# Performance work log

Measured on AMD Instinct MI355X. Metric: run time of the kernel, lower is better.

## Reference

```python
import jax, jax.numpy as jnp
import numpy as np

B, T, P, D, H = 16, 512, 576, 1024, 16
HD = D // H  # head_dim = 64
SCALE = 1.0 / np.sqrt(HD).astype(np.float32)


def _split_heads(x):
    # [B, S, D] -> [B, H, S, HD]
    b, s, _ = x.shape
    return x.reshape(b, s, H, HD).transpose(0, 2, 1, 3)


def _merge_heads(x):
    # [B, H, S, HD] -> [B, S, D]
    b, h, s, hd = x.shape
    return x.transpose(0, 2, 1, 3).reshape(b, s, h * hd)


def _linear(x, w, b):
    # torch nn.Linear: y = x @ W^T + b, W is [out, in]
    return jnp.einsum('bsd,od->bso', x, w) + b


def setup_inputs() -> dict:
    key = jax.random.key(0)
    ks = jax.random.split(key, 12)
    inp = {
        'text_feats': jax.random.normal(ks[0], (B, T, D), jnp.float32),
        'image_feats': jax.random.normal(ks[1], (B, P, D), jnp.float32),
        'text_mask': jnp.ones((B, T), dtype=bool),
    }
    names = ['qt', 'ki', 'vi', 'qi', 'kt', 'vt', 'ot', 'oi']
    for i, n in enumerate(names):
        inp['w_' + n] = jax.random.normal(ks[2 + i], (D, D), jnp.float32) * 0.02
        inp['b_' + n] = jnp.zeros((D,), jnp.float32)
    return inp


def reference(text_feats, image_feats, text_mask,
              w_qt, b_qt, w_ki, b_ki, w_vi, b_vi,
              w_qi, b_qi, w_kt, b_kt, w_vt, b_vt,
              w_ot, b_ot, w_oi, b_oi):
    # ---- text attends to image (no mask on image keys) ----
    q_t = _split_heads(_linear(text_feats, w_qt, b_qt))    # [B,H,T,HD]
    k_i = _split_heads(_linear(image_feats, w_ki, b_ki))   # [B,H,P,HD]
    v_i = _split_heads(_linear(image_feats, w_vi, b_vi))   # [B,H,P,HD]
    scores_ti = jnp.einsum('bhtd,bhpd->bhtp', q_t, k_i) * SCALE
    attn_ti = jax.nn.softmax(scores_ti, axis=-1)
    text_attended = _merge_heads(jnp.einsum('bhtp,bhpd->bhtd', attn_ti, v_i))
    text_attended = _linear(text_attended, w_ot, b_ot)

    # ---- image attends to text (mask on text keys) ----
    q_i = _split_heads(_linear(image_feats, w_qi, b_qi))   # [B,H,P,HD]
    k_t = _split_heads(_linear(text_feats, w_kt, b_kt))    # [B,H,T,HD]
    v_t = _split_heads(_linear(text_feats, w_vt, b_vt))    # [B,H,T,HD]
    scores_it = jnp.einsum('bhpd,bhtd->bhpt', q_i, k_t) * SCALE
    scores_it = jnp.where(text_mask[:, None, None, :], scores_it, -jnp.inf)
    attn_it = jax.nn.softmax(scores_it, axis=-1)
    image_attended = _merge_heads(jnp.einsum('bhpt,bhtd->bhpd', attn_it, v_t))
    image_attended = _linear(image_attended, w_oi, b_oi)

    return (text_attended, image_attended)
```

## Files before the change

### kernel.cpp

```cpp
#include <hip/hip_runtime.h>
#include <stdint.h>

typedef unsigned short u16;
typedef __bf16 bf16x8 __attribute__((ext_vector_type(8)));
typedef float f32x4 __attribute__((ext_vector_type(4)));

#define SCALE_QK 0.125f

__device__ __forceinline__ u16 f2bf(float f) {
    uint32_t u = __builtin_bit_cast(uint32_t, f);
    u += 0x7FFFu + ((u >> 16) & 1u);
    return (u16)(u >> 16);
}

__device__ __forceinline__ int bdiv(int x, int S) {
    return (S == 512) ? (x >> 9) : (int)(((uint64_t)(x >> 6) * 954437177ull) >> 33);
}

__device__ __forceinline__ void gload16(const void* g, void* l) {
    __builtin_amdgcn_global_load_lds(
        (__attribute__((address_space(1))) void*)(g),
        (__attribute__((address_space(3))) void*)(l), 16, 0, 0);
}

template<int W>
__device__ __forceinline__ void vwait() {
    asm volatile("s_waitcnt vmcnt(%0)" :: "n"(W) : "memory");
}

__global__ void cvt_f32_bf16(const float* __restrict__ src, u16* __restrict__ dst, int n4) {
    int i = blockIdx.x * blockDim.x + threadIdx.x;
    if (i >= n4) return;
    float4 v = ((const float4*)src)[i];
    ushort4 o;
    o.x = f2bf(v.x); o.y = f2bf(v.y); o.z = f2bf(v.z); o.w = f2bf(v.w);
    ((ushort4*)dst)[i] = o;
}

struct Ptr8 { const float* p[8]; };

__global__ void cvt_w8(Ptr8 srcs, u16* __restrict__ dst) {
    int i = blockIdx.x * blockDim.x + threadIdx.x;
    int mat = i >> 18, off = i & 262143;
    float4 v = ((const float4*)srcs.p[mat])[off];
    ushort4 o;
    o.x = f2bf(v.x); o.y = f2bf(v.y); o.z = f2bf(v.z); o.w = f2bf(v.w);
    ((ushort4*)(dst + ((size_t)mat << 20)))[off] = o;
}

__global__ void prep(const int* __restrict__ maski, float* __restrict__ mb,
                     const float* __restrict__ bqt, const float* __restrict__ bkt,
                     const float* __restrict__ bqi, const float* __restrict__ bki,
                     float* __restrict__ biasbuf) {
    int i = blockIdx.x * blockDim.x + threadIdx.x;
    if (i < 8192) {
        int v0 = maski[0];
        int v = (v0 == 0x01010101) ? (int)((const unsigned char*)maski)[i] : maski[i];
        mb[i] = v ? 0.0f : -1e30f;
    } else if (i < 12288) {
        int j = i - 8192;
        float v = (j < 1024) ? bqt[j] : (j < 2048) ? bkt[j - 1024]
                : (j < 3072) ? bqi[j - 2048] : bki[j - 3072];
        biasbuf[j] = v;
    }
}

struct Seg {
    const u16* A; const u16* B; const float* bias; void* C;
    int nx, S, layout, end; size_t pstr;
};
struct Segs { Seg s[4]; };

__global__ __launch_bounds__(512, 2)
void gemm256v2(Segs segs) {
    constexpr int K = 1024;
    __shared__ u16 U[4][256 * 64];
    const int tid = threadIdx.x;
    const int wid = tid >> 6, lane = tid & 63;
    const int lo = lane & 15, hi = lane >> 4;
    const int wm = wid >> 2, wn = wid & 3;
    const int tot = (int)gridDim.x;
    int f = ((int)blockIdx.x & 7) * (tot >> 3) + ((int)blockIdx.x >> 3);
    int si = 0;
    while (si < 3 && f >= segs.s[si].end) ++si;
    if (si > 0) f -= segs.s[si - 1].end;
    const Seg sg = segs.s[si];
    const int bm = f / sg.nx, bn = f - bm * sg.nx;
    const u16* Ab = sg.A + (size_t)bm * 256 * K;
    const u16* Bb = sg.B + (size_t)bn * 256 * K;

    const int srow8 = tid >> 3;
    const int sslot = tid & 7;

    auto stage_unit = [&](int u) {
        const int reg = u & 3;
        const int kb = u * 32;
#pragma unroll
        for (int c = 0; c < 4; ++c) {
            int row = c * 64 + srow8;
            int ss = sslot ^ (row & 7);
            const u16* src = (ss < 4)
                ? Ab + (size_t)row * K + kb + ss * 8
                : Bb + (size_t)row * K + kb + (ss - 4) * 8;
            gload16(src, &U[reg][0] + c * 4096 + wid * 512);
        }
    };

    f32x4 acc[8][4] = {};

    stage_unit(0); stage_unit(1); stage_unit(2);

    auto phase = [&](int u, bool doStage) {
        const u16* R = &U[u & 3][0];
        bf16x8 af[8], bq[4];
#pragma unroll
        for (int m = 0; m < 8; ++m) {
            int row = wm * 128 + m * 16 + lo;
            af[m] = *(const bf16x8*)(R + row * 64 + ((hi ^ (row & 7)) << 3));
        }
#pragma unroll
        for (int n = 0; n < 4; ++n) {
            int row = wn * 64 + n * 16 + lo;
            bq[n] = *(const bf16x8*)(R + row * 64 + (((4 + hi) ^ (row & 7)) << 3));
        }
        if (doStage) stage_unit(u + 3);
        __builtin_amdgcn_s_setprio(1);
#pragma unroll
        for (int m = 0; m < 8; ++m)
#pragma unroll
            for (int n = 0; n < 4; ++n)
                acc[m][n] = __builtin_amdgcn_mfma_f32_16x16x32_bf16(af[m], bq[n], acc[m][n], 0, 0, 0);
        __builtin_amdgcn_s_setprio(0);
    };

#pragma unroll 4
    for (int u = 0; u < 28; ++u) {
        vwait<8>();
        __builtin_amdgcn_s_barrier();
        phase(u, true);
    }
    vwait<8>(); __builtin_amdgcn_s_barrier(); phase(28, true);
    vwait<8>(); __builtin_amdgcn_s_barrier(); phase(29, false);
    vwait<4>(); __builtin_amdgcn_s_barrier(); phase(30, false);
    vwait<0>(); __builtin_amdgcn_s_barrier(); phase(31, false);

    const int rowbase = bm * 256 + wm * 128, colbase = bn * 256 + wn * 64;

    if (sg.layout == 0) {
        float* C = (float*)sg.C;
#pragma unroll
        for (int m = 0; m < 8; ++m)
#pragma unroll
            for (int r = 0; r < 4; ++r) {
                int row = rowbase + m * 16 + hi * 4 + r;
#pragma unroll
                for (int n = 0; n < 4; ++n) {
                    int col = colbase + n * 16 + lo;
                    C[(size_t)row * 1024 + col] = acc[m][n][r] + sg.bias[col];
                }
            }
    } else if (sg.layout == 1) {
#pragma unroll
        for (int m = 0; m < 8; ++m)
#pragma unroll
            for (int r = 0; r < 4; ++r) {
                int row = rowbase + m * 16 + hi * 4 + r;
                int b = bdiv(row, sg.S);
                int s = row - b * sg.S;
#pragma unroll
                for (int n = 0; n < 4; ++n) {
                    int cb = colbase + n * 16;
                    int part = cb >> 10, h = (cb >> 6) & 15;
                    u16* bp = (u16*)sg.C + (size_t)part * sg.pstr +
                              (((size_t)(b * 16 + h) * sg.S + s) << 6) + (cb & 63) + lo;
                    *bp = f2bf(acc[m][n][r] + sg.bias[cb + lo]);
                }
            }
    } else {
        u16* base = (u16*)sg.C;
        int bn_[4], s0_[4];
#pragma unroll
        for (int n = 0; n < 4; ++n) {
            int col0 = colbase + n * 16;
            int b = bdiv(col0, sg.S);
            bn_[n] = b;
            s0_[n] = col0 - b * sg.S;
        }
#pragma unroll
        for (int m = 0; m < 8; ++m)
#pragma unroll
            for (int r = 0; r < 4; ++r) {
                int dout = rowbase + m * 16 + hi * 4 + r;
                float bv = sg.bias[dout];
#pragma unroll
                for (int n = 0; n < 4; ++n)
                    base[((size_t)bn_[n] * 1024 + dout) * sg.S + s0_[n] + lo] =
                        f2bf(acc[m][n][r] + bv);
            }
    }
}

template<int MASKED, int NQ, int SK>
__global__ __launch_bounds__(256)
void attn_v4(const u16* __restrict__ Q, const u16* __restrict__ Kb,
             const u16* __restrict__ Vt, const float* __restrict__ mb,
             u16* __restrict__ Out) {
    constexpr int SQ = NQ * 64;
    constexpr int NC = SK / 64;
    __shared__ u16 kls[2][64 * 64];
    __shared__ u16 vls[2][64 * 64];
    __shared__ u16 pls[4][16 * 72];
    const int tid = threadIdx.x, wid = tid >> 6, lane = tid & 63;
    const int lo = lane & 15, hi = lane >> 4;
    const int id = blockIdx.x;
    const int f = (id & 7) * (NQ * 32) + (id >> 3);
    const int qc = f % NQ, bh = f / NQ;
    const int b = bh >> 4, h = bh & 15;
    const int q0 = qc * 64 + wid * 16;
    const u16* Qp = Q + ((size_t)bh * SQ + q0) * 64;
    const u16* Kp = Kb + (size_t)bh * SK * 64;
    const u16* Vp = Vt + (size_t)bh * 64 * SK;

    bf16x8 qf[2];
#pragma unroll
    for (int ks = 0; ks < 2; ++ks)
        qf[ks] = *(const bf16x8*)(Qp + lo * 64 + ks * 32 + hi * 8);

    f32x4 oacc[4] = {};
    float m = -3e38f, l = 0.f;
    u16* pl = pls[wid];
    uint32_t* pl32 = (uint32_t*)pl;

    auto stage = [&](int bufi, int c0) {
#pragma unroll
        for (int j = 0; j < 2; ++j) {
            const int beta = (j * 4 + wid) * 64 + lane;
            const int row = beta >> 3, slot = beta & 7;
            const int e = (slot ^ (row & 7)) << 3;
            gload16(Kp + (size_t)(c0 + row) * 64 + e,
                    &kls[bufi][0] + (j * 4 + wid) * 512);
            gload16(Vp + (size_t)row * SK + c0 + e,
                    &vls[bufi][0] + (j * 4 + wid) * 512);
        }
    };

    stage(0, 0);
    __syncthreads();

    for (int c = 0; c < NC; ++c) {
        const int c0 = c * 64;
        if (c + 1 < NC) stage((c + 1) & 1, c0 + 64);
        const u16* kb = &kls[c & 1][0];
        const u16* vb = &vls[c & 1][0];

        float sc[4][4];
#pragma unroll
        for (int kt = 0; kt < 4; ++kt) {
            const int krow = kt * 16 + lo;
            const int rx = krow & 7;
            bf16x8 kf0 = *(const bf16x8*)(kb + krow * 64 + ((hi ^ rx) << 3));
            bf16x8 kf1 = *(const bf16x8*)(kb + krow * 64 + (((4 + hi) ^ rx) << 3));
            f32x4 z = {};
            __builtin_amdgcn_s_setprio(1);
            z = __builtin_amdgcn_mfma_f32_16x16x32_bf16(kf0, qf[0], z, 0, 0, 0);
            z = __builtin_amdgcn_mfma_f32_16x16x32_bf16(kf1, qf[1], z, 0, 0, 0);
            __builtin_amdgcn_s_setprio(0);
            if (MASKED) {
                float4 mv = *(const float4*)(mb + b * SK + c0 + kt * 16 + hi * 4);
#pragma unroll
                for (int r = 0; r < 4; ++r) sc[kt][r] = z[r] * SCALE_QK + ((const float*)&mv)[r];
            } else {
#pragma unroll
                for (int r = 0; r < 4; ++r) sc[kt][r] = z[r] * SCALE_QK;
            }
        }
        float a0 = fmaxf(fmaxf(sc[0][0], sc[0][1]), fmaxf(sc[0][2], sc[0][3]));
        float a1 = fmaxf(fmaxf(sc[1][0], sc[1][1]), fmaxf(sc[1][2], sc[1][3]));
        float a2 = fmaxf(fmaxf(sc[2][0], sc[2][1]), fmaxf(sc[2][2], sc[2][3]));
        float a3 = fmaxf(fmaxf(sc[3][0], sc[3][1]), fmaxf(sc[3][2], sc[3][3]));
        float pmax = fmaxf(fmaxf(a0, a1), fmaxf(a2, a3));
        pmax = fmaxf(pmax, __shfl_xor(pmax, 16));
        pmax = fmaxf(pmax, __shfl_xor(pmax, 32));
        if (!__all(pmax - m <= 8.0f)) {
            float mn = fmaxf(m, pmax);
            float alpha = __expf(m - mn);
            m = mn;
            l *= alpha;
#pragma unroll
            for (int n = 0; n < 4; ++n)
#pragma unroll
                for (int r = 0; r < 4; ++r) oacc[n][r] *= alpha;
        }
        float sum = 0.f;
#pragma unroll
        for (int kt = 0; kt < 4; ++kt) {
#pragma unroll
            for (int r = 0; r < 4; ++r) {
                float p = __expf(sc[kt][r] - m);
                sc[kt][r] = p;
                sum += p;
            }
        }
        sum += __shfl_xor(sum, 16);
        sum += __shfl_xor(sum, 32);
        l += sum;
#pragma unroll
        for (int kt = 0; kt < 4; ++kt) {
#pragma unroll
            for (int rp = 0; rp < 2; ++rp) {
                uint32_t w = (uint32_t)f2bf(sc[kt][2 * rp]) |
                             ((uint32_t)f2bf(sc[kt][2 * rp + 1]) << 16);
                pl32[lo * 36 + kt * 8 + hi * 2 + rp] = w;
            }
        }
        bf16x8 pf0 = *(const bf16x8*)(pl + lo * 72 + hi * 8);
        bf16x8 pf1 = *(const bf16x8*)(pl + lo * 72 + 32 + hi * 8);
        __builtin_amdgcn_s_setprio(1);
#pragma unroll
        for (int n = 0; n < 4; ++n) {
            const int d = n * 16 + lo;
            const int dx = d & 7;
            bf16x8 v0 = *(const bf16x8*)(vb + d * 64 + ((hi ^ dx) << 3));
            bf16x8 v1 = *(const bf16x8*)(vb + d * 64 + (((4 + hi) ^ dx) << 3));
            oacc[n] = __builtin_amdgcn_mfma_f32_16x16x32_bf16(v0, pf0, oacc[n], 0, 0, 0);
            oacc[n] = __builtin_amdgcn_mfma_f32_16x16x32_bf16(v1, pf1, oacc[n], 0, 0, 0);
        }
        __builtin_amdgcn_s_setprio(0);
        __syncthreads();
    }
    const float inv = 1.0f / l;
    u16* op = Out + ((size_t)(b * SQ + q0 + lo)) * 1024 + h * 64;
#pragma unroll
    for (int n = 0; n < 4; ++n) {
        ushort4 w;
        w.x = f2bf(oacc[n][0] * inv);
        w.y = f2bf(oacc[n][1] * inv);
        w.z = f2bf(oacc[n][2] * inv);
        w.w = f2bf(oacc[n][3] * inv);
        *(ushort4*)(op + n * 16 + hi * 4) = w;
    }
}

extern "C" void kernel_launch(void* const* d_in, const int* in_sizes, int n_in,
                              void* d_out, int out_size, void* d_ws, size_t ws_size,
                              hipStream_t stream) {
    (void)in_sizes; (void)n_in; (void)out_size; (void)ws_size;
    const float* text  = (const float*)d_in[0];
    const float* image = (const float*)d_in[1];
    const int*   maski = (const int*)d_in[2];
    const float* w_qt = (const float*)d_in[3];  const float* b_qt = (const float*)d_in[4];
    const float* w_ki = (const float*)d_in[5];  const float* b_ki = (const float*)d_in[6];
    const float* w_vi = (const float*)d_in[7];  const float* b_vi = (const float*)d_in[8];
    const float* w_qi = (const float*)d_in[9];  const float* b_qi = (const float*)d_in[10];
    const float* w_kt = (const float*)d_in[11]; const float* b_kt = (const float*)d_in[12];
    const float* w_vt = (const float*)d_in[13]; const float* b_vt = (const float*)d_in[14];
    const float* w_ot = (const float*)d_in[15]; const float* b_ot = (const float*)d_in[16];
    const float* w_oi = (const float*)d_in[17]; const float* b_oi = (const float*)d_in[18];

    const int B = 16, T = 512, P = 576, D = 1024;
    const int MT = B * T;
    const int MI = B * P;
    const size_t M1 = 1 << 20;

    char* wp = (char*)d_ws;
    auto alloc = [&](size_t bytes) { char* r = wp; wp += (bytes + 255) & ~(size_t)255; return r; };
    u16* Xt   = (u16*)alloc((size_t)MT * D * 2);
    u16* Xi   = (u16*)alloc((size_t)MI * D * 2);
    u16* Wall = (u16*)alloc(8 * M1 * 2);
    float* biasbuf = (float*)alloc(4096 * 4);
    float* mbf  = (float*)alloc((size_t)B * T * 4);
    u16* QKt  = (u16*)alloc((size_t)2 * MT * D * 2);
    u16* QKi  = (u16*)alloc((size_t)2 * MI * D * 2);
    u16* Vtt  = (u16*)alloc((size_t)MT * D * 2);
    u16* Vti  = (u16*)alloc((size_t)MI * D * 2);

    const u16* Wqk_t = Wall;
    const u16* Wqk_i = Wall + 2 * M1;
    const u16* Wv_t  = Wall + 4 * M1;
    const u16* Wv_i  = Wall + 5 * M1;
    const u16* Wot   = Wall + 6 * M1;
    const u16* Woi   = Wall + 7 * M1;

    cvt_f32_bf16<<<(MT * D / 4) / 256, 256, 0, stream>>>(text, Xt, MT * D / 4);
    cvt_f32_bf16<<<(MI * D / 4) / 256, 256, 0, stream>>>(image, Xi, MI * D / 4);
    Ptr8 w8 = {{w_qt, w_kt, w_qi, w_ki, w_vt, w_vi, w_ot, w_oi}};
    cvt_w8<<<8192, 256, 0, stream>>>(w8, Wall);
    prep<<<48, 256, 0, stream>>>(maski, mbf, b_qt, b_kt, b_qi, b_ki, biasbuf);

    {
        Segs sgs;
        sgs.s[0] = {Xt,   Wqk_t, biasbuf,        QKt, 8,  512, 1, 256, (size_t)MT * D};
        sgs.s[1] = {Xi,   Wqk_i, biasbuf + 2048, QKi, 8,  576, 1, 544, (size_t)MI * D};
        sgs.s[2] = {Wv_t, Xt,    b_vt,           Vtt, 32, 512, 2, 672, 0};
        sgs.s[3] = {Wv_i, Xi,    b_vi,           Vti, 36, 576, 2, 816, 0};
        gemm256v2<<<816, 512, 0, stream>>>(sgs);
    }

    attn_v4<0, 8, 576><<<8 * 256, 256, 0, stream>>>(
        QKt, QKi + (size_t)MI * D, Vti, nullptr, Xt);
    attn_v4<1, 9, 512><<<9 * 256, 256, 0, stream>>>(
        QKi, QKt + (size_t)MT * D, Vtt, mbf, Xi);

    {
        Segs sgs;
        sgs.s[0] = {Xt, Wot, b_ot, d_out, 4, 512, 0, 128, 0};
        sgs.s[1] = {Xi, Woi, b_oi, (void*)((float*)d_out + (size_t)MT * D), 4, 576, 0, 272, 0};
        sgs.s[2] = sgs.s[1]; sgs.s[2].end = 272;
        sgs.s[3] = sgs.s[1]; sgs.s[3].end = 272;
        gemm256v2<<<272, 512, 0, stream>>>(sgs);
    }
}
```

Before: 358.3 us.

## Restructure GEMM mainloop to double-buffered 64-wide K tiles with split stages

Replaces the 4-stage ring of 32-wide K units (A and B packed in one buffer) with separate A and B double buffers holding 64-wide K tiles. Each tile is consumed in four sub-phases, with the next tile's loads spread across them. This halves the pipeline depth, drops the minimum-occupancy launch bound, and halves the A fragment registers per phase. It adds more barriers per tile and gives less prefetch lead time, which may expose global load latency.

```diff
diff --git a/kernel.cpp b/kernel.cpp
--- a/kernel.cpp
+++ b/kernel.cpp
@@ -71,10 +71,12 @@
 };
 struct Segs { Seg s[4]; };
 
-__global__ __launch_bounds__(512, 2)
-void gemm256v2(Segs segs) {
+__global__ __launch_bounds__(512)
+void gemm256v3(Segs segs) {
     constexpr int K = 1024;
-    __shared__ u16 U[4][256 * 64];
+    constexpr int NT = 16;
+    __shared__ u16 As[2][256 * 64];
+    __shared__ u16 Bs[2][256 * 64];
     const int tid = threadIdx.x;
     const int wid = tid >> 6, lane = tid & 63;
     const int lo = lane & 15, hi = lane >> 4;
@@ -89,60 +91,71 @@
     const u16* Ab = sg.A + (size_t)bm * 256 * K;
     const u16* Bb = sg.B + (size_t)bn * 256 * K;
 
-    const int srow8 = tid >> 3;
+    const int srow = tid >> 3;
     const int sslot = tid & 7;
 
-    auto stage_unit = [&](int u) {
-        const int reg = u & 3;
-        const int kb = u * 32;
-#pragma unroll
-        for (int c = 0; c < 4; ++c) {
-            int row = c * 64 + srow8;
-            int ss = sslot ^ (row & 7);
-            const u16* src = (ss < 4)
-                ? Ab + (size_t)row * K + kb + ss * 8
-                : Bb + (size_t)row * K + kb + (ss - 4) * 8;
-            gload16(src, &U[reg][0] + c * 4096 + wid * 512);
-        }
+    auto stageA = [&](int buf, int t1, int c) {
+        int row = c * 64 + srow;
+        int ss = sslot ^ (row & 7);
+        gload16(Ab + (size_t)row * K + t1 * 64 + ss * 8,
+                &As[buf][0] + c * 4096 + wid * 512);
     };
+    auto stageB = [&](int buf, int t1, int c) {
+        int row = c * 64 + srow;
+        int ss = sslot ^ (row & 7);
+        gload16(Bb + (size_t)row * K + t1 * 64 + ss * 8,
+                &Bs[buf][0] + c * 4096 + wid * 512);
+    };
 
     f32x4 acc[8][4] = {};
 
-    stage_unit(0); stage_unit(1); stage_unit(2);
-
-    auto phase = [&](int u, bool doStage) {
-        const u16* R = &U[u & 3][0];
-        bf16x8 af[8], bq[4];
-#pragma unroll
-        for (int m = 0; m < 8; ++m) {
-            int row = wm * 128 + m * 16 + lo;
-            af[m] = *(const bf16x8*)(R + row * 64 + ((hi ^ (row & 7)) << 3));
-        }
-#pragma unroll
-        for (int n = 0; n < 4; ++n) {
-            int row = wn * 64 + n * 16 + lo;
-            bq[n] = *(const bf16x8*)(R + row * 64 + (((4 + hi) ^ (row & 7)) << 3));
-        }
-        if (doStage) stage_unit(u + 3);
-        __builtin_amdgcn_s_setprio(1);
-#pragma unroll
-        for (int m = 0; m < 8; ++m)
-#pragma unroll
-            for (int n = 0; n < 4; ++n)
-                acc[m][n] = __builtin_amdgcn_mfma_f32_16x16x32_bf16(af[m], bq[n], acc[m][n], 0, 0, 0);
-        __builtin_amdgcn_s_setprio(0);
-    };
-
-#pragma unroll 4
-    for (int u = 0; u < 28; ++u) {
-        vwait<8>();
-        __builtin_amdgcn_s_barrier();
-        phase(u, true);
-    }
-    vwait<8>(); __builtin_amdgcn_s_barrier(); phase(28, true);
-    vwait<8>(); __builtin_amdgcn_s_barrier(); phase(29, false);
-    vwait<4>(); __builtin_amdgcn_s_barrier(); phase(30, false);
-    vwait<0>(); __builtin_amdgcn_s_barrier(); phase(31, false);
+    stageB(0, 0, 0); stageB(0, 0, 1); stageB(0, 0, 2); stageB(0, 0, 3);
+    stageA(0, 0, 0); stageA(0, 0, 2); stageA(0, 0, 1); stageA(0, 0, 3);
+    vwait<2>();
+    __builtin_amdgcn_s_barrier();
+
+    for (int t = 0; t < NT; ++t) {
+        const int cur = t & 1;
+        const u16* At = &As[cur][0];
+        const u16* Bt = &Bs[cur][0];
+        const bool st = (t + 1 < NT);
+#pragma unroll
+        for (int ph = 0; ph < 4; ++ph) {
+            const int ks = ph >> 1, mh = ph & 1;
+            bf16x8 af[4], bq[4];
+#pragma unroll
+            for (int m = 0; m < 4; ++m) {
+                int row = wm * 128 + mh * 64 + m * 16 + lo;
+                af[m] = *(const bf16x8*)(At + row * 64 + (((ks * 4 + hi) ^ (row & 7)) << 3));
+            }
+#pragma unroll
+            for (int n = 0; n < 4; ++n) {
+                int row = wn * 64 + n * 16 + lo;
+                bq[n] = *(const bf16x8*)(Bt + row * 64 + (((ks * 4 + hi) ^ (row & 7)) << 3));
+            }
+            if (st) {
+                if (ph == 0)      { stageB(cur ^ 1, t + 1, 0); stageB(cur ^ 1, t + 1, 1); }
+                else if (ph == 1) { stageB(cur ^ 1, t + 1, 2); stageB(cur ^ 1, t + 1, 3); }
+                else if (ph == 2) { stageA(cur ^ 1, t + 1, 0); stageA(cur ^ 1, t + 1, 2); }
+                else              { stageA(cur ^ 1, t + 1, 1); stageA(cur ^ 1, t + 1, 3); }
+            }
+            __builtin_amdgcn_s_barrier();
+            __builtin_amdgcn_s_setprio(1);
+#pragma unroll
+            for (int m = 0; m < 4; ++m)
+#pragma unroll
+                for (int n = 0; n < 4; ++n)
+                    acc[mh * 4 + m][n] =
+                        __builtin_amdgcn_mfma_f32_16x16x32_bf16(af[m], bq[n], acc[mh * 4 + m][n], 0, 0, 0);
+            __builtin_amdgcn_s_setprio(0);
+            if (ph == 0) {
+                if (st) vwait<2>(); else vwait<0>();
+            } else if (ph == 3) {
+                vwait<2>();
+            }
+            __builtin_amdgcn_s_barrier();
+        }
+    }
 
     const int rowbase = bm * 256 + wm * 128, colbase = bn * 256 + wn * 64;
 
@@ -393,7 +406,7 @@
         sgs.s[1] = {Xi,   Wqk_i, biasbuf + 2048, QKi, 8,  576, 1, 544, (size_t)MI * D};
         sgs.s[2] = {Wv_t, Xt,    b_vt,           Vtt, 32, 512, 2, 672, 0};
         sgs.s[3] = {Wv_i, Xi,    b_vi,           Vti, 36, 576, 2, 816, 0};
-        gemm256v2<<<816, 512, 0, stream>>>(sgs);
+        gemm256v3<<<816, 512, 0, stream>>>(sgs);
     }
 
     attn_v4<0, 8, 576><<<8 * 256, 256, 0, stream>>>(
@@ -407,6 +420,6 @@
         sgs.s[1] = {Xi, Woi, b_oi, (void*)((float*)d_out + (size_t)MT * D), 4, 576, 0, 272, 0};
         sgs.s[2] = sgs.s[1]; sgs.s[2].end = 272;
         sgs.s[3] = sgs.s[1]; sgs.s[3].end = 272;
-        gemm256v2<<<272, 512, 0, stream>>>(sgs);
-    }
-}
+        gemm256v3<<<272, 512, 0, stream>>>(sgs);
+    }
+}
```

After: 377.4 us. 5.3% more time.

## Restructure GEMM main loop into double-buffered pairs with precomputed addresses

Applied to the files above, without the earlier changes.

The GEMM pipeline changes from a 4-slot ring with three stages in flight and partial vmcnt waits to a pair-based double buffer. Each step waits for all loads, computes two K-slices, and issues loads for the next pair between them. Global source pointers and LDS read offsets are now computed once instead of per unit, which cuts address arithmetic. The min-blocks-per-CU hint of 2 is also dropped. Waiting on vmcnt(0) every step leaves less load overlap than the old deeper prefetch, so memory latency may be less well hidden.

```diff
diff --git a/kernel.cpp b/kernel.cpp
--- a/kernel.cpp
+++ b/kernel.cpp
@@ -71,10 +71,10 @@
 };
 struct Segs { Seg s[4]; };
 
-__global__ __launch_bounds__(512, 2)
-void gemm256v2(Segs segs) {
+__global__ __launch_bounds__(512)
+void gemm256v4(Segs segs) {
     constexpr int K = 1024;
-    __shared__ u16 U[4][256 * 64];
+    __shared__ u16 U[4][16384];
     const int tid = threadIdx.x;
     const int wid = tid >> 6, lane = tid & 63;
     const int lo = lane & 15, hi = lane >> 4;
@@ -89,41 +89,50 @@
     const u16* Ab = sg.A + (size_t)bm * 256 * K;
     const u16* Bb = sg.B + (size_t)bn * 256 * K;
 
-    const int srow8 = tid >> 3;
-    const int sslot = tid & 7;
-
-    auto stage_unit = [&](int u) {
-        const int reg = u & 3;
-        const int kb = u * 32;
+    const int srow = tid >> 3;
+    const int ss = (tid & 7) ^ (srow & 7);
+    const u16* baseC[4];
+#pragma unroll
+    for (int c = 0; c < 4; ++c) {
+        int row = c * 64 + srow;
+        baseC[c] = (ss < 4) ? Ab + (size_t)row * K + ss * 8
+                            : Bb + (size_t)row * K + (ss - 4) * 8;
+    }
+    u16* const U0 = &U[0][0];
+    u16* const ldsD[4] = { U0 + 0 * 4096 + wid * 512, U0 + 1 * 4096 + wid * 512,
+                           U0 + 2 * 4096 + wid * 512, U0 + 3 * 4096 + wid * 512 };
+
+    auto stagePair = [&](int regBase) {
 #pragma unroll
         for (int c = 0; c < 4; ++c) {
-            int row = c * 64 + srow8;
-            int ss = sslot ^ (row & 7);
-            const u16* src = (ss < 4)
-                ? Ab + (size_t)row * K + kb + ss * 8
-                : Bb + (size_t)row * K + kb + (ss - 4) * 8;
-            gload16(src, &U[reg][0] + c * 4096 + wid * 512);
-        }
+            gload16(baseC[c],      ldsD[c] + regBase * 16384);
+            gload16(baseC[c] + 32, ldsD[c] + (regBase + 1) * 16384);
+        }
+#pragma unroll
+        for (int c = 0; c < 4; ++c) baseC[c] += 64;
     };
 
+    int afo[8], bqo[4];
+#pragma unroll
+    for (int m = 0; m < 8; ++m) {
+        int row = wm * 128 + m * 16 + lo;
+        afo[m] = row * 64 + ((hi ^ (row & 7)) << 3);
+    }
+#pragma unroll
+    for (int n = 0; n < 4; ++n) {
+        int row = wn * 64 + n * 16 + lo;
+        bqo[n] = row * 64 + (((4 + hi) ^ (row & 7)) << 3);
+    }
+
     f32x4 acc[8][4] = {};
 
-    stage_unit(0); stage_unit(1); stage_unit(2);
-
-    auto phase = [&](int u, bool doStage) {
-        const u16* R = &U[u & 3][0];
+    auto compute = [&](int reg) {
+        const u16* R = U0 + reg * 16384;
         bf16x8 af[8], bq[4];
 #pragma unroll
-        for (int m = 0; m < 8; ++m) {
-            int row = wm * 128 + m * 16 + lo;
-            af[m] = *(const bf16x8*)(R + row * 64 + ((hi ^ (row & 7)) << 3));
-        }
-#pragma unroll
-        for (int n = 0; n < 4; ++n) {
-            int row = wn * 64 + n * 16 + lo;
-            bq[n] = *(const bf16x8*)(R + row * 64 + (((4 + hi) ^ (row & 7)) << 3));
-        }
-        if (doStage) stage_unit(u + 3);
+        for (int m = 0; m < 8; ++m) af[m] = *(const bf16x8*)(R + afo[m]);
+#pragma unroll
+        for (int n = 0; n < 4; ++n) bq[n] = *(const bf16x8*)(R + bqo[n]);
         __builtin_amdgcn_s_setprio(1);
 #pragma unroll
         for (int m = 0; m < 8; ++m)
@@ -133,16 +142,15 @@
         __builtin_amdgcn_s_setprio(0);
     };
 
-#pragma unroll 4
-    for (int u = 0; u < 28; ++u) {
-        vwait<8>();
+    stagePair(0);
+#pragma unroll 2
+    for (int p = 0; p < 16; ++p) {
+        vwait<0>();
         __builtin_amdgcn_s_barrier();
-        phase(u, true);
-    }
-    vwait<8>(); __builtin_amdgcn_s_barrier(); phase(28, true);
-    vwait<8>(); __builtin_amdgcn_s_barrier(); phase(29, false);
-    vwait<4>(); __builtin_amdgcn_s_barrier(); phase(30, false);
-    vwait<0>(); __builtin_amdgcn_s_barrier(); phase(31, false);
+        compute(2 * (p & 1));
+        if (p < 15) stagePair((p & 1) ? 0 : 2);
+        compute(2 * (p & 1) + 1);
+    }
 
     const int rowbase = bm * 256 + wm * 128, colbase = bn * 256 + wn * 64;
 
@@ -393,7 +401,7 @@
         sgs.s[1] = {Xi,   Wqk_i, biasbuf + 2048, QKi, 8,  576, 1, 544, (size_t)MI * D};
         sgs.s[2] = {Wv_t, Xt,    b_vt,           Vtt, 32, 512, 2, 672, 0};
         sgs.s[3] = {Wv_i, Xi,    b_vi,           Vti, 36, 576, 2, 816, 0};
-        gemm256v2<<<816, 512, 0, stream>>>(sgs);
+        gemm256v4<<<816, 512, 0, stream>>>(sgs);
     }
 
     attn_v4<0, 8, 576><<<8 * 256, 256, 0, stream>>>(
@@ -407,6 +415,6 @@
         sgs.s[1] = {Xi, Woi, b_oi, (void*)((float*)d_out + (size_t)MT * D), 4, 576, 0, 272, 0};
         sgs.s[2] = sgs.s[1]; sgs.s[2].end = 272;
         sgs.s[3] = sgs.s[1]; sgs.s[3].end = 272;
-        gemm256v2<<<272, 512, 0, stream>>>(sgs);
-    }
-}
+        gemm256v4<<<272, 512, 0, stream>>>(sgs);
+    }
+}
```

Result: slower. 426.5 us (+19.0%).
